# Kernel optimization log

Hardware: AMD Instinct MI355X
Metric: run time of the kernel (lower is better)

## Reference

```python
import jax, jax.numpy as jnp
import numpy as np

N, E, D_IN, D, H, L, D_EMB, T = 4096, 131072, 72, 256, 8, 2, 128, 5
HD = D // H
LN_EPS = 1e-5


def _linear(x, w, b):
    # torch Linear: w is [out, in]
    return x @ w.T + b


def _layernorm(x, g, b):
    mu = jnp.mean(x, axis=-1, keepdims=True)
    var = jnp.var(x, axis=-1, keepdims=True)
    return (x - mu) * jax.lax.rsqrt(var + LN_EPS) * g + b


def _gps_layer(x, edge_index, p):
    src, dst = edge_index[0], edge_index[1]
    # GINConv: sum-aggregate neighbor messages, then MLP((1+eps)*x + agg)
    agg = jax.ops.segment_sum(x[src], dst, num_segments=N)
    h = (1.0 + p['gin_eps']) * x + agg
    h = _linear(jax.nn.elu(_linear(h, p['mlp_w1'], p['mlp_b1'])), p['mlp_w2'], p['mlp_b2'])
    h = jax.nn.elu(_layernorm(h, p['ln1_g'], p['ln1_b']))
    x = x + h

    # global multi-head self-attention over all N nodes (seq len = N)
    qkv = x @ p['attn_in_w'].T + p['attn_in_b']  # [N, 3D]
    q, k, v = jnp.split(qkv, 3, axis=-1)
    q = q.reshape(N, H, HD)
    k = k.reshape(N, H, HD)
    v = v.reshape(N, H, HD)
    scores = jnp.einsum('nhd,mhd->hnm', q, k) / np.sqrt(HD).astype(np.float32)
    attn = jax.nn.softmax(scores, axis=-1)
    o = jnp.einsum('hnm,mhd->nhd', attn, v).reshape(N, D)
    o = _linear(o, p['attn_out_w'], p['attn_out_b'])
    o = _layernorm(o, p['ln2_g'], p['ln2_b'])
    x = x + o

    # FFN (dim -> 2*dim -> dim, GELU)
    f = _linear(jax.nn.gelu(_linear(x, p['ffn_w1'], p['ffn_b1'])), p['ffn_w2'], p['ffn_b2'])
    f = _layernorm(f, p['ln3_g'], p['ln3_b'])
    return x + f


def setup_inputs() -> dict:
    key = jax.random.key(0)
    ks = iter(jax.random.split(key, 64))

    def w(shape, fan_in):
        return jax.random.normal(next(ks), shape, jnp.float32) * (1.0 / np.sqrt(fan_in))

    inp = {
        'x': jax.random.normal(next(ks), (N, D_IN), jnp.float32),
        'edge_index': jax.random.randint(next(ks), (2, E), 0, N, jnp.int64),
        'in_w': w((D, D_IN), D_IN), 'in_b': jnp.zeros((D,), jnp.float32),
        'head_w1': w((D_EMB, D), D), 'head_b1': jnp.zeros((D_EMB,), jnp.float32),
        'head_w2': w((T, D_EMB), D_EMB), 'head_b2': jnp.zeros((T,), jnp.float32),
    }
    # stacked per-layer params, leading axis L
    inp['mlp_w1'] = w((L, D, D), D); inp['mlp_b1'] = jnp.zeros((L, D), jnp.float32)
    inp['mlp_w2'] = w((L, D, D), D); inp['mlp_b2'] = jnp.zeros((L, D), jnp.float32)
    inp['gin_eps'] = jnp.zeros((L,), jnp.float32)
    inp['ln1_g'] = jnp.ones((L, D), jnp.float32); inp['ln1_b'] = jnp.zeros((L, D), jnp.float32)
    inp['attn_in_w'] = w((L, 3 * D, D), D); inp['attn_in_b'] = jnp.zeros((L, 3 * D), jnp.float32)
    inp['attn_out_w'] = w((L, D, D), D); inp['attn_out_b'] = jnp.zeros((L, D), jnp.float32)
    inp['ln2_g'] = jnp.ones((L, D), jnp.float32); inp['ln2_b'] = jnp.zeros((L, D), jnp.float32)
    inp['ffn_w1'] = w((L, 2 * D, D), D); inp['ffn_b1'] = jnp.zeros((L, 2 * D), jnp.float32)
    inp['ffn_w2'] = w((L, D, 2 * D), 2 * D); inp['ffn_b2'] = jnp.zeros((L, D), jnp.float32)
    inp['ln3_g'] = jnp.ones((L, D), jnp.float32); inp['ln3_b'] = jnp.zeros((L, D), jnp.float32)
    return inp


PER_LAYER = ['mlp_w1', 'mlp_b1', 'mlp_w2', 'mlp_b2', 'gin_eps', 'ln1_g', 'ln1_b',
             'attn_in_w', 'attn_in_b', 'attn_out_w', 'attn_out_b', 'ln2_g', 'ln2_b',
             'ffn_w1', 'ffn_b1', 'ffn_w2', 'ffn_b2', 'ln3_g', 'ln3_b']


def reference(x, edge_index, in_w, in_b, head_w1, head_b1, head_w2, head_b2,
              mlp_w1, mlp_b1, mlp_w2, mlp_b2, gin_eps, ln1_g, ln1_b,
              attn_in_w, attn_in_b, attn_out_w, attn_out_b, ln2_g, ln2_b,
              ffn_w1, ffn_b1, ffn_w2, ffn_b2, ln3_g, ln3_b):
    stacked = dict(mlp_w1=mlp_w1, mlp_b1=mlp_b1, mlp_w2=mlp_w2, mlp_b2=mlp_b2,
                   gin_eps=gin_eps, ln1_g=ln1_g, ln1_b=ln1_b,
                   attn_in_w=attn_in_w, attn_in_b=attn_in_b,
                   attn_out_w=attn_out_w, attn_out_b=attn_out_b,
                   ln2_g=ln2_g, ln2_b=ln2_b, ffn_w1=ffn_w1, ffn_b1=ffn_b1,
                   ffn_w2=ffn_w2, ffn_b2=ffn_b2, ln3_g=ln3_g, ln3_b=ln3_b)
    h = jax.nn.elu(_linear(x, in_w, in_b))  # input_proj (dropout/noise off in eval)
    for l in range(L):
        p = {k: v[l] for k, v in stacked.items()}
        h = _gps_layer(h, edge_index, p)
    out = _linear(jax.nn.elu(_linear(h, head_w1, head_b1)), head_w2, head_b2)
    return out
```

## Files before the change

### kernel.cpp

```cpp
#include <hip/hip_runtime.h>
#include <math.h>

#define NN 4096
#define NE 131072
#define DIM 256
#define NHEAD 8
#define HD 32

typedef __attribute__((ext_vector_type(8))) short short8v;
typedef __attribute__((ext_vector_type(4))) float f32x4;
#define MFMA16(a, b, c) __builtin_amdgcn_mfma_f32_16x16x32_bf16(a, b, c, 0, 0, 0)

__device__ __forceinline__ float elu_f(float v){ return v > 0.f ? v : expm1f(v); }
__device__ __forceinline__ float gelu_f(float v){
  const float c = 0.7978845608028654f;
  float t = tanhf(c * (v + 0.044715f * v * v * v));
  return 0.5f * v * (1.f + t);
}
__device__ __forceinline__ unsigned short f2bf(float f) {
  unsigned int u = __builtin_bit_cast(unsigned int, f);
  u += 0x7FFFu + ((u >> 16) & 1u);
  return (unsigned short)(u >> 16);
}
__device__ __forceinline__ unsigned int pk2(float a, float b) {
  return (unsigned int)f2bf(a) | ((unsigned int)f2bf(b) << 16);
}

__global__ void zero_counts(int* __restrict__ counts) {
  int i = blockIdx.x * 256 + threadIdx.x;
  if (i < NN) counts[i] = 0;
}

__global__ void count_edges(const int* __restrict__ ei, int* __restrict__ counts) {
  int e = blockIdx.x * 256 + threadIdx.x;
  if (e < NE) atomicAdd(&counts[ei[NE + e]], 1);
}

__global__ __launch_bounds__(1024) void scan_offsets(const int* __restrict__ counts,
                                                     int* __restrict__ offs,
                                                     int* __restrict__ cursor) {
  __shared__ int tmp[1024];
  int t = threadIdx.x;
  int base = t * 4;
  int c0 = counts[base], c1 = counts[base+1], c2 = counts[base+2], c3 = counts[base+3];
  int tsum = c0 + c1 + c2 + c3;
  tmp[t] = tsum;
  __syncthreads();
  for (int d = 1; d < 1024; d <<= 1) {
    int v = (t >= d) ? tmp[t - d] : 0;
    __syncthreads();
    tmp[t] += v;
    __syncthreads();
  }
  int excl = tmp[t] - tsum;
  offs[base]   = excl;           cursor[base]   = excl;
  offs[base+1] = excl + c0;      cursor[base+1] = excl + c0;
  offs[base+2] = excl + c0 + c1; cursor[base+2] = excl + c0 + c1;
  offs[base+3] = excl + c0 + c1 + c2; cursor[base+3] = excl + c0 + c1 + c2;
  if (t == 1023) offs[NN] = tmp[1023];
}

__global__ void scatter_edges(const int* __restrict__ ei, int* __restrict__ cursor,
                              int* __restrict__ esrc) {
  int e = blockIdx.x * 256 + threadIdx.x;
  if (e < NE) {
    int d = ei[NE + e];
    int pos = atomicAdd(&cursor[d], 1);
    esrc[pos] = ei[e];
  }
}

__global__ __launch_bounds__(256) void gin_agg(const int* __restrict__ offs,
                                               const int* __restrict__ esrc,
                                               const float* __restrict__ x,
                                               const float* __restrict__ eps_p, int l,
                                               unsigned short* __restrict__ aggb) {
  int n = blockIdx.x, c = threadIdx.x;
  int e0 = offs[n], e1 = offs[n + 1];
  float acc = 0.f;
  for (int e = e0; e < e1; e++) acc += x[(size_t)esrc[e] * DIM + c];
  float eps = eps_p[l];
  aggb[(size_t)n * DIM + c] = f2bf((1.f + eps) * x[(size_t)n * DIM + c] + acc);
}

template<int ACT, int WF32, int WBF16, int QSCALE>
__global__ __launch_bounds__(256) void gemm_mfma(
    const unsigned short* __restrict__ A, const unsigned short* __restrict__ W,
    const float* __restrict__ bias, float* __restrict__ Cf,
    unsigned short* __restrict__ Cb, int M, int N, int K)
{
  __shared__ __align__(16) unsigned short As[64][40];
  __shared__ __align__(16) unsigned short Ws[64][40];
  int t = threadIdx.x;
  int w = t >> 6, lane = t & 63, lo = lane & 15, g = lane >> 4;
  int wr = w >> 1, wc = w & 1;
  int bn = blockIdx.x * 64, bm = blockIdx.y * 64;
  int srow = t >> 2, skk = (t & 3) << 3;
  const unsigned short* ap = A + (size_t)(bm + srow) * K + skk;
  const unsigned short* wp = W + (size_t)(bn + srow) * K + skk;

  f32x4 acc[2][2] = {{{0.f,0.f,0.f,0.f},{0.f,0.f,0.f,0.f}},
                     {{0.f,0.f,0.f,0.f},{0.f,0.f,0.f,0.f}}};

  for (int k0 = 0; k0 < K; k0 += 32) {
    *(short8v*)&As[srow][skk] = *(const short8v*)(ap + k0);
    *(short8v*)&Ws[srow][skk] = *(const short8v*)(wp + k0);
    __syncthreads();
    short8v a0 = *(const short8v*)&As[wr * 32 + lo][8 * g];
    short8v a1 = *(const short8v*)&As[wr * 32 + 16 + lo][8 * g];
    short8v b0 = *(const short8v*)&Ws[wc * 32 + lo][8 * g];
    short8v b1 = *(const short8v*)&Ws[wc * 32 + 16 + lo][8 * g];
    acc[0][0] = MFMA16(a0, b0, acc[0][0]);
    acc[0][1] = MFMA16(a0, b1, acc[0][1]);
    acc[1][0] = MFMA16(a1, b0, acc[1][0]);
    acc[1][1] = MFMA16(a1, b1, acc[1][1]);
    __syncthreads();
  }

  #pragma unroll
  for (int mi = 0; mi < 2; mi++) {
    #pragma unroll
    for (int ni = 0; ni < 2; ni++) {
      #pragma unroll
      for (int r = 0; r < 4; r++) {
        int row = bm + wr * 32 + mi * 16 + 4 * g + r;
        int col = bn + wc * 32 + ni * 16 + lo;
        float v = acc[mi][ni][r] + bias[col];
        if (ACT == 1) v = elu_f(v);
        if (ACT == 2) v = gelu_f(v);
        if (QSCALE) { if (col < 256) v *= 0.17677669529663687f; }
        if (WF32) Cf[(size_t)row * N + col] = v;
        if (WBF16) Cb[(size_t)row * N + col] = f2bf(v);
      }
    }
  }
}

template<int ACT>
__global__ __launch_bounds__(256) void ln_act_add(const float* __restrict__ in,
                                                  const float* __restrict__ g,
                                                  const float* __restrict__ b,
                                                  float* __restrict__ x,
                                                  unsigned short* __restrict__ xb) {
  int rowb = blockIdx.x;
  int c = threadIdx.x;
  float v = in[(size_t)rowb * DIM + c];
  float s = v, s2 = v * v;
  #pragma unroll
  for (int off = 32; off >= 1; off >>= 1) {
    s  += __shfl_xor(s,  off, 64);
    s2 += __shfl_xor(s2, off, 64);
  }
  __shared__ float ws1[4], ws2[4];
  int w = threadIdx.x >> 6, lane = threadIdx.x & 63;
  if (lane == 0) { ws1[w] = s; ws2[w] = s2; }
  __syncthreads();
  s  = ws1[0] + ws1[1] + ws1[2] + ws1[3];
  s2 = ws2[0] + ws2[1] + ws2[2] + ws2[3];
  float mean = s * (1.f / DIM);
  float var = s2 * (1.f / DIM) - mean * mean;
  float r = rsqrtf(var + 1e-5f);
  float o = (v - mean) * r * g[c] + b[c];
  if (ACT == 1) o = elu_f(o);
  float nx = x[(size_t)rowb * DIM + c] + o;
  x[(size_t)rowb * DIM + c] = nx;
  xb[(size_t)rowb * DIM + c] = f2bf(nx);
}

__global__ __launch_bounds__(256) void vt_transpose(const unsigned short* __restrict__ tbb,
                                                    unsigned short* __restrict__ VT) {
  __shared__ unsigned short lds[128][33];
  int h = blockIdx.y;
  int nb = blockIdx.x * 128;
  int tid = threadIdx.x;
  int r8 = tid >> 5, d = tid & 31;
  #pragma unroll
  for (int i = 0; i < 16; i++) {
    int n = i * 8 + r8;
    lds[n][d] = tbb[(size_t)(nb + n) * 768 + 512 + h * 32 + d];
  }
  __syncthreads();
  int dd = tid >> 7, j = tid & 127;
  #pragma unroll
  for (int i = 0; i < 16; i++) {
    int d2 = i * 2 + dd;
    VT[((size_t)h * 32 + d2) * 4096 + nb + j] = lds[j][d2];
  }
}

__global__ __launch_bounds__(256) void attn_mfma_split(
    const unsigned short* __restrict__ qkvb, const unsigned short* __restrict__ VT,
    float* __restrict__ po, float* __restrict__ ml, int kspan) {
  __shared__ __align__(16) unsigned short Ks[2][64][40];
  __shared__ __align__(16) unsigned short Vs[2][32][72];
  int tid = threadIdx.x;
  int w = tid >> 6, lane = tid & 63;
  int lo = lane & 15, g = lane >> 4;
  int h = blockIdx.y;
  int s = blockIdx.z;
  int qb = blockIdx.x * 64 + w * 16;
  int k_lo = s * kspan, k_hi = k_lo + kspan;

  int krow = tid >> 2, kq = (tid & 3) * 8;
  int vrow = tid >> 3, vo = (tid & 7) * 8;
  const unsigned short* Kg = qkvb + 256 + h * 32;
  const unsigned short* Vg = VT + ((size_t)(h * 32 + vrow)) * 4096;

  short8v qf = *(const short8v*)(qkvb + (size_t)(qb + lo) * 768 + h * 32 + 8 * g);

  f32x4 acc0 = {0.f, 0.f, 0.f, 0.f};
  f32x4 acc1 = {0.f, 0.f, 0.f, 0.f};
  float m = -1e30f, l = 0.f;
  const f32x4 zf = {0.f, 0.f, 0.f, 0.f};

  {
    short8v rk0 = *(const short8v*)(Kg + (size_t)(k_lo + krow) * 768 + kq);
    short8v rv0 = *(const short8v*)(Vg + k_lo + vo);
    *(short8v*)&Ks[0][krow][kq] = rk0;
    *(short8v*)&Vs[0][vrow][vo] = rv0;
  }
  __syncthreads();

  int buf = 0;
  for (int kb = k_lo; kb < k_hi; kb += 64) {
    short8v rk, rv;
    bool more = (kb + 64 < k_hi);
    if (more) {
      rk = *(const short8v*)(Kg + (size_t)(kb + 64 + krow) * 768 + kq);
      rv = *(const short8v*)(Vg + kb + 64 + vo);
    }

    short8v kA0 = *(const short8v*)&Ks[buf][lo][8 * g];
    short8v kA1 = *(const short8v*)&Ks[buf][16 + lo][8 * g];
    short8v kA2 = *(const short8v*)&Ks[buf][32 + lo][8 * g];
    short8v kA3 = *(const short8v*)&Ks[buf][48 + lo][8 * g];
    f32x4 s0_ = MFMA16(kA0, qf, zf);
    f32x4 s1_ = MFMA16(kA1, qf, zf);
    f32x4 s2_ = MFMA16(kA2, qf, zf);
    f32x4 s3_ = MFMA16(kA3, qf, zf);

    float ta_ = fmaxf(fmaxf(fmaxf(s0_[0],s0_[1]), fmaxf(s0_[2],s0_[3])),
                      fmaxf(fmaxf(s1_[0],s1_[1]), fmaxf(s1_[2],s1_[3])));
    float tb_ = fmaxf(fmaxf(fmaxf(s2_[0],s2_[1]), fmaxf(s2_[2],s2_[3])),
                      fmaxf(fmaxf(s3_[0],s3_[1]), fmaxf(s3_[2],s3_[3])));
    float t_ = fmaxf(ta_, tb_);
    t_ = fmaxf(t_, __shfl_xor(t_, 16, 64));
    t_ = fmaxf(t_, __shfl_xor(t_, 32, 64));
    if (!__all(t_ <= m)) {
      float nm_ = fmaxf(m, t_);
      float f_ = __expf(m - nm_);
      m = nm_; l *= f_;
      acc0[0]*=f_; acc0[1]*=f_; acc0[2]*=f_; acc0[3]*=f_;
      acc1[0]*=f_; acc1[1]*=f_; acc1[2]*=f_; acc1[3]*=f_;
    }
    float p0_=__expf(s0_[0]-m), p1_=__expf(s0_[1]-m), p2_=__expf(s0_[2]-m), p3_=__expf(s0_[3]-m);
    float p4_=__expf(s1_[0]-m), p5_=__expf(s1_[1]-m), p6_=__expf(s1_[2]-m), p7_=__expf(s1_[3]-m);
    float p8_=__expf(s2_[0]-m), p9_=__expf(s2_[1]-m), pA_=__expf(s2_[2]-m), pB_=__expf(s2_[3]-m);
    float pC_=__expf(s3_[0]-m), pD_=__expf(s3_[1]-m), pE_=__expf(s3_[2]-m), pF_=__expf(s3_[3]-m);
    l += ((((p0_+p1_)+(p2_+p3_)) + ((p4_+p5_)+(p6_+p7_))) +
          (((p8_+p9_)+(pA_+pB_)) + ((pC_+pD_)+(pE_+pF_))));

    uint4 uA_ = { pk2(p0_,p1_), pk2(p2_,p3_), pk2(p4_,p5_), pk2(p6_,p7_) };
    uint4 uB_ = { pk2(p8_,p9_), pk2(pA_,pB_), pk2(pC_,pD_), pk2(pE_,pF_) };
    short8v pbA_ = __builtin_bit_cast(short8v, uA_);
    short8v pbB_ = __builtin_bit_cast(short8v, uB_);

    short4 Wa0 = *(const short4*)&Vs[buf][lo][4 * g];
    short4 Wa1 = *(const short4*)&Vs[buf][lo][16 + 4 * g];
    short4 Wa2 = *(const short4*)&Vs[buf][lo][32 + 4 * g];
    short4 Wa3 = *(const short4*)&Vs[buf][lo][48 + 4 * g];
    short4 Xa0 = *(const short4*)&Vs[buf][16 + lo][4 * g];
    short4 Xa1 = *(const short4*)&Vs[buf][16 + lo][16 + 4 * g];
    short4 Xa2 = *(const short4*)&Vs[buf][16 + lo][32 + 4 * g];
    short4 Xa3 = *(const short4*)&Vs[buf][16 + lo][48 + 4 * g];
    short8v va0_ = {Wa0.x,Wa0.y,Wa0.z,Wa0.w, Wa1.x,Wa1.y,Wa1.z,Wa1.w};
    short8v va1_ = {Wa2.x,Wa2.y,Wa2.z,Wa2.w, Wa3.x,Wa3.y,Wa3.z,Wa3.w};
    short8v vb0_ = {Xa0.x,Xa0.y,Xa0.z,Xa0.w, Xa1.x,Xa1.y,Xa1.z,Xa1.w};
    short8v vb1_ = {Xa2.x,Xa2.y,Xa2.z,Xa2.w, Xa3.x,Xa3.y,Xa3.z,Xa3.w};
    acc0 = MFMA16(va0_, pbA_, acc0);
    acc0 = MFMA16(va1_, pbB_, acc0);
    acc1 = MFMA16(vb0_, pbA_, acc1);
    acc1 = MFMA16(vb1_, pbB_, acc1);

    if (more) {
      *(short8v*)&Ks[buf ^ 1][krow][kq] = rk;
      *(short8v*)&Vs[buf ^ 1][vrow][vo] = rv;
    }
    __syncthreads();
    buf ^= 1;
  }

  l += __shfl_xor(l, 16, 64);
  l += __shfl_xor(l, 32, 64);

  int q = qb + lo;
  float* pr = po + ((size_t)s * NN + q) * DIM + h * 32 + 4 * g;
  *(f32x4*)pr = acc0;
  *(f32x4*)(pr + 16) = acc1;
  if (g == 0) {
    float2* mlp = (float2*)(ml + (((size_t)s * NN + q) * NHEAD + h) * 2);
    *mlp = float2{m, l};
  }
}

__global__ __launch_bounds__(256) void attn_merge(const float* __restrict__ po,
                                                  const float* __restrict__ ml,
                                                  unsigned short* __restrict__ attb, int S) {
  int q = blockIdx.x;
  int c = threadIdx.x;
  int h = c >> 5;
  float M = -1e30f;
  for (int s = 0; s < S; s++)
    M = fmaxf(M, ml[(((size_t)s * NN + q) * NHEAD + h) * 2]);
  float L = 0.f, O = 0.f;
  for (int s = 0; s < S; s++) {
    const float* mlp = ml + (((size_t)s * NN + q) * NHEAD + h) * 2;
    float e = __expf(mlp[0] - M);
    L += e * mlp[1];
    O += e * po[((size_t)s * NN + q) * DIM + c];
  }
  attb[(size_t)q * DIM + c] = f2bf(O / L);
}

#define WO0 0
#define WO1 131072
#define WO2 262144
#define WO3 655360
#define WO4 786432
#define WO5 1048576
#define WO6 1310720
#define WTOT 1343488
__global__ __launch_bounds__(256) void wconv(const float* __restrict__ s0, const float* __restrict__ s1,
                                             const float* __restrict__ s2, const float* __restrict__ s3,
                                             const float* __restrict__ s4, const float* __restrict__ s5,
                                             const float* __restrict__ s6, unsigned short* __restrict__ dst) {
  int i4 = (blockIdx.x * 256 + threadIdx.x) * 4;
  if (i4 >= WTOT) return;
  const float* src; int loc;
  if      (i4 < WO1) { src = s0; loc = i4 - WO0; }
  else if (i4 < WO2) { src = s1; loc = i4 - WO1; }
  else if (i4 < WO3) { src = s2; loc = i4 - WO2; }
  else if (i4 < WO4) { src = s3; loc = i4 - WO3; }
  else if (i4 < WO5) { src = s4; loc = i4 - WO4; }
  else if (i4 < WO6) { src = s5; loc = i4 - WO5; }
  else               { src = s6; loc = i4 - WO6; }
  float4 v = *(const float4*)(src + loc);
  ushort4 o;
  o.x = f2bf(v.x); o.y = f2bf(v.y); o.z = f2bf(v.z); o.w = f2bf(v.w);
  *(ushort4*)(dst + i4) = o;
}

__global__ __launch_bounds__(256) void pad72_96(const float* __restrict__ src,
                                                unsigned short* __restrict__ dst, int total) {
  int idx = blockIdx.x * 256 + threadIdx.x;
  if (idx >= total) return;
  int row = idx / 96, col = idx - row * 96;
  dst[idx] = (col < 72) ? f2bf(src[row * 72 + col]) : (unsigned short)0;
}

__global__ void head2_kernel(const float* __restrict__ e, const float* __restrict__ w,
                             const float* __restrict__ b, float* __restrict__ out) {
  int idx = blockIdx.x * 256 + threadIdx.x;
  if (idx >= NN * 5) return;
  int rowi = idx / 5, col = idx % 5;
  float s = b[col];
  const float* ep = e + (size_t)rowi * 128;
  const float* wp = w + (size_t)col * 128;
  #pragma unroll 16
  for (int k = 0; k < 128; k++) s += ep[k] * wp[k];
  out[idx] = s;
}

extern "C" void kernel_launch(void* const* d_in, const int* in_sizes, int n_in,
                              void* d_out, int out_size, void* d_ws, size_t ws_size,
                              hipStream_t stream) {
  const float* x_in   = (const float*)d_in[0];
  const int*   ei     = (const int*)  d_in[1];
  const float* in_w   = (const float*)d_in[2];
  const float* in_b   = (const float*)d_in[3];
  const float* head_w1= (const float*)d_in[4];
  const float* head_b1= (const float*)d_in[5];
  const float* head_w2= (const float*)d_in[6];
  const float* head_b2= (const float*)d_in[7];
  const float* mlp_w1 = (const float*)d_in[8];
  const float* mlp_b1 = (const float*)d_in[9];
  const float* mlp_w2 = (const float*)d_in[10];
  const float* mlp_b2 = (const float*)d_in[11];
  const float* gin_eps= (const float*)d_in[12];
  const float* ln1_g  = (const float*)d_in[13];
  const float* ln1_b  = (const float*)d_in[14];
  const float* attn_in_w = (const float*)d_in[15];
  const float* attn_in_b = (const float*)d_in[16];
  const float* attn_out_w= (const float*)d_in[17];
  const float* attn_out_b= (const float*)d_in[18];
  const float* ln2_g  = (const float*)d_in[19];
  const float* ln2_b  = (const float*)d_in[20];
  const float* ffn_w1 = (const float*)d_in[21];
  const float* ffn_b1 = (const float*)d_in[22];
  const float* ffn_w2 = (const float*)d_in[23];
  const float* ffn_b2 = (const float*)d_in[24];
  const float* ln3_g  = (const float*)d_in[25];
  const float* ln3_b  = (const float*)d_in[26];

  float* ws = (float*)d_ws;
  float* x    = ws;
  float* t2   = x  + (size_t)NN * DIM;
  float* he   = t2 + (size_t)NN * DIM;
  unsigned short* xb   = (unsigned short*)(he + (size_t)NN * 128);
  unsigned short* tbb  = xb   + (size_t)NN * DIM;
  unsigned short* aggb = tbb  + (size_t)NN * 768;
  unsigned short* attb = aggb + (size_t)NN * DIM;
  unsigned short* VT   = attb + (size_t)NN * DIM;
  unsigned short* xinb = VT   + (size_t)NN * DIM;
  unsigned short* inwb = xinb + (size_t)NN * 96;
  unsigned short* warena = inwb + 256 * 96;
  int* counts = (int*)(warena + WTOT);
  int* offs   = counts + NN;
  int* cursor = offs + NN + 1;
  int* esrc   = cursor + NN;
  float* po   = (float*)(esrc + NE);
  size_t used_f = (size_t)(po - ws);
  int S = 1;
  for (int cand = 4; cand >= 2; cand >>= 1) {
    size_t need = (used_f + (size_t)cand * NN * DIM + (size_t)cand * NN * NHEAD * 2) * 4;
    if (ws_size >= need) { S = cand; break; }
  }
  float* ml = po + (size_t)S * NN * DIM;
  int kspan = NN / S;

  const unsigned short* w_mlp1 = warena + WO0;
  const unsigned short* w_mlp2 = warena + WO1;
  const unsigned short* w_qkv  = warena + WO2;
  const unsigned short* w_aout = warena + WO3;
  const unsigned short* w_ffn1 = warena + WO4;
  const unsigned short* w_ffn2 = warena + WO5;
  const unsigned short* w_h1   = warena + WO6;

  zero_counts<<<16, 256, 0, stream>>>(counts);
  count_edges<<<NE / 256, 256, 0, stream>>>(ei, counts);
  scan_offsets<<<1, 1024, 0, stream>>>(counts, offs, cursor);
  scatter_edges<<<NE / 256, 256, 0, stream>>>(ei, cursor, esrc);

  wconv<<<1312, 256, 0, stream>>>(mlp_w1, mlp_w2, attn_in_w, attn_out_w, ffn_w1, ffn_w2,
                                  head_w1, warena);
  pad72_96<<<(NN * 96 + 255) / 256, 256, 0, stream>>>(x_in, xinb, NN * 96);
  pad72_96<<<(256 * 96 + 255) / 256, 256, 0, stream>>>(in_w, inwb, 256 * 96);

  gemm_mfma<1,1,1,0><<<dim3(DIM/64, NN/64), 256, 0, stream>>>(xinb, inwb, in_b, x, xb,
                                                              NN, DIM, 96);

  for (int l = 0; l < 2; l++) {
    gin_agg<<<NN, 256, 0, stream>>>(offs, esrc, x, gin_eps, l, aggb);
    gemm_mfma<1,0,1,0><<<dim3(4, 64), 256, 0, stream>>>(aggb, w_mlp1 + (size_t)l*65536,
                                                        mlp_b1 + l*DIM, nullptr, tbb,
                                                        NN, DIM, DIM);
    gemm_mfma<0,1,0,0><<<dim3(4, 64), 256, 0, stream>>>(tbb, w_mlp2 + (size_t)l*65536,
                                                        mlp_b2 + l*DIM, t2, nullptr,
                                                        NN, DIM, DIM);
    ln_act_add<1><<<NN, 256, 0, stream>>>(t2, ln1_g + l*DIM, ln1_b + l*DIM, x, xb);

    gemm_mfma<0,0,1,1><<<dim3(12, 64), 256, 0, stream>>>(xb, w_qkv + (size_t)l*196608,
                                                         attn_in_b + l*768, nullptr, tbb,
                                                         NN, 768, DIM);
    vt_transpose<<<dim3(32, 8), 256, 0, stream>>>(tbb, VT);
    attn_mfma_split<<<dim3(64, NHEAD, S), 256, 0, stream>>>(tbb, VT, po, ml, kspan);
    attn_merge<<<NN, 256, 0, stream>>>(po, ml, attb, S);
    gemm_mfma<0,1,0,0><<<dim3(4, 64), 256, 0, stream>>>(attb, w_aout + (size_t)l*65536,
                                                        attn_out_b + l*DIM, t2, nullptr,
                                                        NN, DIM, DIM);
    ln_act_add<0><<<NN, 256, 0, stream>>>(t2, ln2_g + l*DIM, ln2_b + l*DIM, x, xb);

    gemm_mfma<2,0,1,0><<<dim3(8, 64), 256, 0, stream>>>(xb, w_ffn1 + (size_t)l*131072,
                                                        ffn_b1 + l*512, nullptr, tbb,
                                                        NN, 512, DIM);
    gemm_mfma<0,1,0,0><<<dim3(4, 64), 256, 0, stream>>>(tbb, w_ffn2 + (size_t)l*131072,
                                                        ffn_b2 + l*DIM, t2, nullptr,
                                                        NN, DIM, 512);
    ln_act_add<0><<<NN, 256, 0, stream>>>(t2, ln3_g + l*DIM, ln3_b + l*DIM, x, xb);
  }

  gemm_mfma<1,1,0,0><<<dim3(2, 64), 256, 0, stream>>>(xb, w_h1, head_b1, he, nullptr,
                                                      NN, 128, DIM);
  head2_kernel<<<(NN * 5 + 255) / 256, 256, 0, stream>>>(he, head_w2, head_b2, (float*)d_out);
}
```

Measured before the change: 363.7 us.

## Gather bf16 features in GIN, widen GEMM K-tile, fuse prep conversions

The GIN aggregation now gathers neighbour rows from the bf16 copy of x instead of fp32, halving gather traffic at some precision cost for the residual term. The GEMM kernel gains a BK template parameter, and most GEMMs use a K-tile of 64, which halves the number of barrier-synchronised iterations. The weight conversion and the two padding kernels are merged into one launch to cut launch overhead.

```diff
diff --git a/kernel.cpp b/kernel.cpp
--- a/kernel.cpp
+++ b/kernel.cpp
@@ -21,6 +21,9 @@
   unsigned int u = __builtin_bit_cast(unsigned int, f);
   u += 0x7FFFu + ((u >> 16) & 1u);
   return (unsigned short)(u >> 16);
+}
+__device__ __forceinline__ float bf2f(unsigned short u) {
+  return __builtin_bit_cast(float, (unsigned int)u << 16);
 }
 __device__ __forceinline__ unsigned int pk2(float a, float b) {
   return (unsigned int)f2bf(a) | ((unsigned int)f2bf(b) << 16);
@@ -72,48 +75,56 @@
 
 __global__ __launch_bounds__(256) void gin_agg(const int* __restrict__ offs,
                                                const int* __restrict__ esrc,
-                                               const float* __restrict__ x,
+                                               const unsigned short* __restrict__ xb,
                                                const float* __restrict__ eps_p, int l,
                                                unsigned short* __restrict__ aggb) {
   int n = blockIdx.x, c = threadIdx.x;
   int e0 = offs[n], e1 = offs[n + 1];
   float acc = 0.f;
-  for (int e = e0; e < e1; e++) acc += x[(size_t)esrc[e] * DIM + c];
+  for (int e = e0; e < e1; e++) acc += bf2f(xb[(size_t)esrc[e] * DIM + c]);
   float eps = eps_p[l];
-  aggb[(size_t)n * DIM + c] = f2bf((1.f + eps) * x[(size_t)n * DIM + c] + acc);
-}
-
-template<int ACT, int WF32, int WBF16, int QSCALE>
+  aggb[(size_t)n * DIM + c] = f2bf((1.f + eps) * bf2f(xb[(size_t)n * DIM + c]) + acc);
+}
+
+template<int ACT, int WF32, int WBF16, int QSCALE, int BK>
 __global__ __launch_bounds__(256) void gemm_mfma(
     const unsigned short* __restrict__ A, const unsigned short* __restrict__ W,
     const float* __restrict__ bias, float* __restrict__ Cf,
     unsigned short* __restrict__ Cb, int M, int N, int K)
 {
-  __shared__ __align__(16) unsigned short As[64][40];
-  __shared__ __align__(16) unsigned short Ws[64][40];
+  __shared__ __align__(16) unsigned short As[64][BK + 8];
+  __shared__ __align__(16) unsigned short Ws[64][BK + 8];
   int t = threadIdx.x;
   int w = t >> 6, lane = t & 63, lo = lane & 15, g = lane >> 4;
   int wr = w >> 1, wc = w & 1;
   int bn = blockIdx.x * 64, bm = blockIdx.y * 64;
-  int srow = t >> 2, skk = (t & 3) << 3;
-  const unsigned short* ap = A + (size_t)(bm + srow) * K + skk;
-  const unsigned short* wp = W + (size_t)(bn + srow) * K + skk;
+  int srow = t >> 2;
+  int sc = (BK == 64) ? (t & 3) * 16 : (t & 3) * 8;
+  const unsigned short* ap = A + (size_t)(bm + srow) * K + sc;
+  const unsigned short* wp = W + (size_t)(bn + srow) * K + sc;
 
   f32x4 acc[2][2] = {{{0.f,0.f,0.f,0.f},{0.f,0.f,0.f,0.f}},
                      {{0.f,0.f,0.f,0.f},{0.f,0.f,0.f,0.f}}};
 
-  for (int k0 = 0; k0 < K; k0 += 32) {
-    *(short8v*)&As[srow][skk] = *(const short8v*)(ap + k0);
-    *(short8v*)&Ws[srow][skk] = *(const short8v*)(wp + k0);
+  for (int k0 = 0; k0 < K; k0 += BK) {
+    *(short8v*)&As[srow][sc] = *(const short8v*)(ap + k0);
+    *(short8v*)&Ws[srow][sc] = *(const short8v*)(wp + k0);
+    if (BK == 64) {
+      *(short8v*)&As[srow][sc + 8] = *(const short8v*)(ap + k0 + 8);
+      *(short8v*)&Ws[srow][sc + 8] = *(const short8v*)(wp + k0 + 8);
+    }
     __syncthreads();
-    short8v a0 = *(const short8v*)&As[wr * 32 + lo][8 * g];
-    short8v a1 = *(const short8v*)&As[wr * 32 + 16 + lo][8 * g];
-    short8v b0 = *(const short8v*)&Ws[wc * 32 + lo][8 * g];
-    short8v b1 = *(const short8v*)&Ws[wc * 32 + 16 + lo][8 * g];
-    acc[0][0] = MFMA16(a0, b0, acc[0][0]);
-    acc[0][1] = MFMA16(a0, b1, acc[0][1]);
-    acc[1][0] = MFMA16(a1, b0, acc[1][0]);
-    acc[1][1] = MFMA16(a1, b1, acc[1][1]);
+    #pragma unroll
+    for (int ks = 0; ks < BK; ks += 32) {
+      short8v a0 = *(const short8v*)&As[wr * 32 + lo][ks + 8 * g];
+      short8v a1 = *(const short8v*)&As[wr * 32 + 16 + lo][ks + 8 * g];
+      short8v b0 = *(const short8v*)&Ws[wc * 32 + lo][ks + 8 * g];
+      short8v b1 = *(const short8v*)&Ws[wc * 32 + 16 + lo][ks + 8 * g];
+      acc[0][0] = MFMA16(a0, b0, acc[0][0]);
+      acc[0][1] = MFMA16(a0, b1, acc[0][1]);
+      acc[1][0] = MFMA16(a1, b0, acc[1][0]);
+      acc[1][1] = MFMA16(a1, b1, acc[1][1]);
+    }
     __syncthreads();
   }
 
@@ -330,32 +341,41 @@
 #define WO5 1048576
 #define WO6 1310720
 #define WTOT 1343488
-__global__ __launch_bounds__(256) void wconv(const float* __restrict__ s0, const float* __restrict__ s1,
-                                             const float* __restrict__ s2, const float* __restrict__ s3,
-                                             const float* __restrict__ s4, const float* __restrict__ s5,
-                                             const float* __restrict__ s6, unsigned short* __restrict__ dst) {
-  int i4 = (blockIdx.x * 256 + threadIdx.x) * 4;
-  if (i4 >= WTOT) return;
-  const float* src; int loc;
-  if      (i4 < WO1) { src = s0; loc = i4 - WO0; }
-  else if (i4 < WO2) { src = s1; loc = i4 - WO1; }
-  else if (i4 < WO3) { src = s2; loc = i4 - WO2; }
-  else if (i4 < WO4) { src = s3; loc = i4 - WO3; }
-  else if (i4 < WO5) { src = s4; loc = i4 - WO4; }
-  else if (i4 < WO6) { src = s5; loc = i4 - WO5; }
-  else               { src = s6; loc = i4 - WO6; }
-  float4 v = *(const float4*)(src + loc);
-  ushort4 o;
-  o.x = f2bf(v.x); o.y = f2bf(v.y); o.z = f2bf(v.z); o.w = f2bf(v.w);
-  *(ushort4*)(dst + i4) = o;
-}
-
-__global__ __launch_bounds__(256) void pad72_96(const float* __restrict__ src,
-                                                unsigned short* __restrict__ dst, int total) {
-  int idx = blockIdx.x * 256 + threadIdx.x;
-  if (idx >= total) return;
-  int row = idx / 96, col = idx - row * 96;
-  dst[idx] = (col < 72) ? f2bf(src[row * 72 + col]) : (unsigned short)0;
+#define WBLK 1312
+#define XPBLK 1536
+#define WPBLK 96
+__global__ __launch_bounds__(256) void prep_convert(
+    const float* __restrict__ s0, const float* __restrict__ s1,
+    const float* __restrict__ s2, const float* __restrict__ s3,
+    const float* __restrict__ s4, const float* __restrict__ s5,
+    const float* __restrict__ s6, unsigned short* __restrict__ dst,
+    const float* __restrict__ x_in, unsigned short* __restrict__ xinb,
+    const float* __restrict__ in_w, unsigned short* __restrict__ inwb) {
+  int bid = blockIdx.x;
+  if (bid < WBLK) {
+    int i4 = (bid * 256 + threadIdx.x) * 4;
+    if (i4 >= WTOT) return;
+    const float* src; int loc;
+    if      (i4 < WO1) { src = s0; loc = i4 - WO0; }
+    else if (i4 < WO2) { src = s1; loc = i4 - WO1; }
+    else if (i4 < WO3) { src = s2; loc = i4 - WO2; }
+    else if (i4 < WO4) { src = s3; loc = i4 - WO3; }
+    else if (i4 < WO5) { src = s4; loc = i4 - WO4; }
+    else if (i4 < WO6) { src = s5; loc = i4 - WO5; }
+    else               { src = s6; loc = i4 - WO6; }
+    float4 v = *(const float4*)(src + loc);
+    ushort4 o;
+    o.x = f2bf(v.x); o.y = f2bf(v.y); o.z = f2bf(v.z); o.w = f2bf(v.w);
+    *(ushort4*)(dst + i4) = o;
+  } else if (bid < WBLK + XPBLK) {
+    int idx = (bid - WBLK) * 256 + threadIdx.x;
+    int row = idx / 96, col = idx - row * 96;
+    xinb[idx] = (col < 72) ? f2bf(x_in[row * 72 + col]) : (unsigned short)0;
+  } else {
+    int idx = (bid - WBLK - XPBLK) * 256 + threadIdx.x;
+    int row = idx / 96, col = idx - row * 96;
+    inwb[idx] = (col < 72) ? f2bf(in_w[row * 72 + col]) : (unsigned short)0;
+  }
 }
 
 __global__ void head2_kernel(const float* __restrict__ e, const float* __restrict__ w,
@@ -441,45 +461,44 @@
   scan_offsets<<<1, 1024, 0, stream>>>(counts, offs, cursor);
   scatter_edges<<<NE / 256, 256, 0, stream>>>(ei, cursor, esrc);
 
-  wconv<<<1312, 256, 0, stream>>>(mlp_w1, mlp_w2, attn_in_w, attn_out_w, ffn_w1, ffn_w2,
-                                  head_w1, warena);
-  pad72_96<<<(NN * 96 + 255) / 256, 256, 0, stream>>>(x_in, xinb, NN * 96);
-  pad72_96<<<(256 * 96 + 255) / 256, 256, 0, stream>>>(in_w, inwb, 256 * 96);
-
-  gemm_mfma<1,1,1,0><<<dim3(DIM/64, NN/64), 256, 0, stream>>>(xinb, inwb, in_b, x, xb,
-                                                              NN, DIM, 96);
+  prep_convert<<<WBLK + XPBLK + WPBLK, 256, 0, stream>>>(
+      mlp_w1, mlp_w2, attn_in_w, attn_out_w, ffn_w1, ffn_w2, head_w1, warena,
+      x_in, xinb, in_w, inwb);
+
+  gemm_mfma<1,1,1,0,32><<<dim3(DIM/64, NN/64), 256, 0, stream>>>(xinb, inwb, in_b, x, xb,
+                                                                 NN, DIM, 96);
 
   for (int l = 0; l < 2; l++) {
-    gin_agg<<<NN, 256, 0, stream>>>(offs, esrc, x, gin_eps, l, aggb);
-    gemm_mfma<1,0,1,0><<<dim3(4, 64), 256, 0, stream>>>(aggb, w_mlp1 + (size_t)l*65536,
-                                                        mlp_b1 + l*DIM, nullptr, tbb,
-                                                        NN, DIM, DIM);
-    gemm_mfma<0,1,0,0><<<dim3(4, 64), 256, 0, stream>>>(tbb, w_mlp2 + (size_t)l*65536,
-                                                        mlp_b2 + l*DIM, t2, nullptr,
-                                                        NN, DIM, DIM);
+    gin_agg<<<NN, 256, 0, stream>>>(offs, esrc, xb, gin_eps, l, aggb);
+    gemm_mfma<1,0,1,0,64><<<dim3(4, 64), 256, 0, stream>>>(aggb, w_mlp1 + (size_t)l*65536,
+                                                           mlp_b1 + l*DIM, nullptr, tbb,
+                                                           NN, DIM, DIM);
+    gemm_mfma<0,1,0,0,64><<<dim3(4, 64), 256, 0, stream>>>(tbb, w_mlp2 + (size_t)l*65536,
+                                                           mlp_b2 + l*DIM, t2, nullptr,
+                                                           NN, DIM, DIM);
     ln_act_add<1><<<NN, 256, 0, stream>>>(t2, ln1_g + l*DIM, ln1_b + l*DIM, x, xb);
 
-    gemm_mfma<0,0,1,1><<<dim3(12, 64), 256, 0, stream>>>(xb, w_qkv + (size_t)l*196608,
-                                                         attn_in_b + l*768, nullptr, tbb,
-                                                         NN, 768, DIM);
+    gemm_mfma<0,0,1,1,64><<<dim3(12, 64), 256, 0, stream>>>(xb, w_qkv + (size_t)l*196608,
+                                                            attn_in_b + l*768, nullptr, tbb,
+                                                            NN, 768, DIM);
     vt_transpose<<<dim3(32, 8), 256, 0, stream>>>(tbb, VT);
     attn_mfma_split<<<dim3(64, NHEAD, S), 256, 0, stream>>>(tbb, VT, po, ml, kspan);
     attn_merge<<<NN, 256, 0, stream>>>(po, ml, attb, S);
-    gemm_mfma<0,1,0,0><<<dim3(4, 64), 256, 0, stream>>>(attb, w_aout + (size_t)l*65536,
-                                                        attn_out_b + l*DIM, t2, nullptr,
-                                                        NN, DIM, DIM);
+    gemm_mfma<0,1,0,0,64><<<dim3(4, 64), 256, 0, stream>>>(attb, w_aout + (size_t)l*65536,
+                                                           attn_out_b + l*DIM, t2, nullptr,
+                                                           NN, DIM, DIM);
     ln_act_add<0><<<NN, 256, 0, stream>>>(t2, ln2_g + l*DIM, ln2_b + l*DIM, x, xb);
 
-    gemm_mfma<2,0,1,0><<<dim3(8, 64), 256, 0, stream>>>(xb, w_ffn1 + (size_t)l*131072,
-                                                        ffn_b1 + l*512, nullptr, tbb,
-                                                        NN, 512, DIM);
-    gemm_mfma<0,1,0,0><<<dim3(4, 64), 256, 0, stream>>>(tbb, w_ffn2 + (size_t)l*131072,
-                                                        ffn_b2 + l*DIM, t2, nullptr,
-                                                        NN, DIM, 512);
+    gemm_mfma<2,0,1,0,64><<<dim3(8, 64), 256, 0, stream>>>(xb, w_ffn1 + (size_t)l*131072,
+                                                           ffn_b1 + l*512, nullptr, tbb,
+                                                           NN, 512, DIM);
+    gemm_mfma<0,1,0,0,64><<<dim3(4, 64), 256, 0, stream>>>(tbb, w_ffn2 + (size_t)l*131072,
+                                                           ffn_b2 + l*DIM, t2, nullptr,
+                                                           NN, DIM, 512);
     ln_act_add<0><<<NN, 256, 0, stream>>>(t2, ln3_g + l*DIM, ln3_b + l*DIM, x, xb);
   }
 
-  gemm_mfma<1,1,0,0><<<dim3(2, 64), 256, 0, stream>>>(xb, w_h1, head_b1, he, nullptr,
-                                                      NN, 128, DIM);
+  gemm_mfma<1,1,0,0,64><<<dim3(2, 64), 256, 0, stream>>>(xb, w_h1, head_b1, he, nullptr,
+                                                         NN, 128, DIM);
   head2_kernel<<<(NN * 5 + 255) / 256, 256, 0, stream>>>(he, head_w2, head_b2, (float*)d_out);
 }
```

Result: no change. 363.2 us (-0.1%).
